# Kernel optimization log

Measured on AMD Instinct MI355X. Metric: run time of the kernel, lower is better.

Reference implementation:

```python
import jax, jax.numpy as jnp
import numpy as np

B, S, D, H = 2, 2048, 512, 8
DK = D // H  # 64
SCALE = (DK * 2) ** 0.5  # sqrt(2*d_k)


def setup_inputs() -> dict:
    key = jax.random.key(0)
    ks = jax.random.split(key, 10)
    f = lambda k, shape, s=1.0: jax.random.normal(k, shape, dtype=jnp.float32) * s
    return {
        "q_real": f(ks[0], (B, S, D)),
        "k_real": f(ks[1], (B, S, D)),
        "v_real": f(ks[2], (B, S, D)),
        "q_phase": f(ks[3], (B, S, D)),
        "k_phase": f(ks[4], (B, S, D)),
        "v_phase": f(ks[5], (B, S, D)),
        "w_q": f(ks[6], (D, D), 0.02),
        "w_k": f(ks[7], (D, D), 0.02),
        "w_v": f(ks[8], (D, D), 0.02),
        "w_o": f(ks[9], (D, D), 0.02),
        "mask": jnp.ones((B, S, S), dtype=jnp.int32),
    }


def _heads(x, w):
    # [B,S,D] @ [D,D] -> [B,H,S,DK]
    y = x @ w
    return y.reshape(B, -1, H, DK).transpose(0, 2, 1, 3)


def reference(q_real, k_real, v_real, q_phase, k_phase, v_phase,
              w_q, w_k, w_v, w_o, mask):
    qr, kr, vr = _heads(q_real, w_q), _heads(k_real, w_k), _heads(v_real, w_v)
    qp, kp, vp = _heads(q_phase, w_q), _heads(k_phase, w_k), _heads(v_phase, w_v)

    # complex-valued attention scores (continue_complex=False path)
    attn_real = jnp.einsum('bhqd,bhkd->bhqk', qr, kr) - jnp.einsum('bhqd,bhkd->bhqk', qp, kp)
    attn_phase = jnp.einsum('bhqd,bhkd->bhqk', qr, kp) + jnp.einsum('bhqd,bhkd->bhqk', qp, kr)

    attn = jnp.sqrt(attn_real * attn_real + attn_phase * attn_phase) / SCALE
    attn = jnp.where(mask[:, None, :, :] == 0, jnp.float32(-1e9), attn)
    attn = jax.nn.softmax(attn, axis=-1)

    xr = jnp.einsum('bhqk,bhkd->bhqd', attn, vr).transpose(0, 2, 1, 3).reshape(B, -1, D)
    xp = jnp.einsum('bhqk,bhkd->bhqd', attn, vp).transpose(0, 2, 1, 3).reshape(B, -1, D)
    return (xr @ w_o, xp @ w_o)
```

## Files before the change

### kernel.cpp

```cpp
#include <hip/hip_runtime.h>
#include <hip/hip_bf16.h>
#include <stdint.h>

#define Bb 2
#define Ss 2048
#define Dd 512
#define Hh 8
#define DKk 64

#define NROW 4096
#define MAT_E 2097152
#define W_E 262144

typedef __attribute__((ext_vector_type(8))) short short8;
typedef __attribute__((ext_vector_type(4))) float f32x4;

__device__ __forceinline__ unsigned short f2bf(float f) {
  union { float f; uint32_t u; } v; v.f = f;
  uint32_t u = v.u;
  uint32_t r = u + 0x7FFFu + ((u >> 16) & 1u);
  return (unsigned short)(r >> 16);
}

__device__ __forceinline__ void g2l16(const char* g, char* l) {
  __builtin_amdgcn_global_load_lds(
      (const __attribute__((address_space(1))) void*)g,
      (__attribute__((address_space(3))) void*)l, 16, 0, 0);
}

__global__ __launch_bounds__(256) void ck_cvt_in(
    const float* __restrict__ a0, const float* __restrict__ a1,
    const float* __restrict__ a2, const float* __restrict__ a3,
    const float* __restrict__ a4, const float* __restrict__ a5,
    unsigned short* __restrict__ out)
{
  int z = blockIdx.y;
  const float* src = z==0?a0: z==1?a1: z==2?a2: z==3?a3: z==4?a4: a5;
  unsigned short* dst = out + (size_t)z * MAT_E;
  int i = blockIdx.x * 256 + threadIdx.x;
  float4 v = ((const float4*)src)[i];
  unsigned short o[4] = {f2bf(v.x), f2bf(v.y), f2bf(v.z), f2bf(v.w)};
  *((uint2*)(dst + (size_t)i * 4)) = *((uint2*)o);
}

__global__ __launch_bounds__(256) void ck_cvt_wt(
    const float* __restrict__ w0, const float* __restrict__ w1,
    const float* __restrict__ w2, const float* __restrict__ w3,
    unsigned short* __restrict__ out)
{
  int z = blockIdx.y;
  const float* w = z==0?w0: z==1?w1: z==2?w2: w3;
  unsigned short* wt = out + (size_t)z * W_E;
  int t = blockIdx.x * 256 + threadIdx.x;
  int d = t >> 9, k = t & 511;
  wt[t] = f2bf(w[k * 512 + d]);
}

__global__ __launch_bounds__(256) void ck_mask_pack(
    const int* __restrict__ mask, unsigned long long* __restrict__ mb)
{
  size_t i = (size_t)blockIdx.x * 256 + threadIdx.x;
  int v = mask[i];
  unsigned long long bits = __ballot(v != 0);
  if ((threadIdx.x & 63) == 0) mb[i >> 6] = bits;
}

__device__ const size_t PROJ_OFF[6] = {0, 2097152, 8388608, 4194304, 6291456, 10485760};

__global__ __launch_bounds__(256) void ck_proj_gemm(
    const unsigned short* __restrict__ xb,
    const unsigned short* __restrict__ wt,
    unsigned short* __restrict__ proj)
{
  int z = blockIdx.z;
  const char* A = (const char*)(xb + (size_t)z * MAT_E);
  const char* W = (const char*)(wt + (size_t)(z % 3) * W_E);

  int tid = threadIdx.x;
  int wave = tid >> 6, lane = tid & 63;
  int lo = lane & 15, hi = lane >> 4;
  int wr = wave >> 1, wc = wave & 1;
  int m0 = blockIdx.x * 128, n0 = blockIdx.y * 128;

  __shared__ __align__(16) char smem[34816];
  char* A0 = smem;          char* A1 = smem + 8192;
  char* B0 = smem + 16384;  char* B1 = smem + 24576;

  int r0s = tid >> 2,        s0s = (tid & 3) ^ ((r0s >> 1) & 3);
  int c1  = 256 + tid;
  int r1s = c1 >> 2,         s1s = (c1 & 3) ^ ((r1s >> 1) & 3);
  int lb0 = wave * 1024;
  int lb1 = 4096 + wave * 1024;

  auto stage = [&](char* Ax, char* Bx, int k0) {
    g2l16(A + (size_t)(m0 + r0s) * 1024 + k0 * 2 + s0s * 16, Ax + lb0);
    g2l16(A + (size_t)(m0 + r1s) * 1024 + k0 * 2 + s1s * 16, Ax + lb1);
    g2l16(W + (size_t)(n0 + r0s) * 1024 + k0 * 2 + s0s * 16, Bx + lb0);
    g2l16(W + (size_t)(n0 + r1s) * 1024 + k0 * 2 + s1s * 16, Bx + lb1);
  };

  f32x4 acc[4][4];
  #pragma unroll
  for (int mf = 0; mf < 4; ++mf)
    #pragma unroll
    for (int nf = 0; nf < 4; ++nf) acc[mf][nf] = (f32x4){0.f, 0.f, 0.f, 0.f};

  int swz = (hi ^ ((lo >> 1) & 3)) * 16;

  auto compute = [&](const char* Ax, const char* Bx) {
    short8 af[4], bf[4];
    #pragma unroll
    for (int mf = 0; mf < 4; ++mf)
      af[mf] = *(const short8*)(Ax + (wr * 64 + mf * 16 + lo) * 64 + swz);
    #pragma unroll
    for (int nf = 0; nf < 4; ++nf)
      bf[nf] = *(const short8*)(Bx + (wc * 64 + nf * 16 + lo) * 64 + swz);
    #pragma unroll
    for (int mf = 0; mf < 4; ++mf)
      #pragma unroll
      for (int nf = 0; nf < 4; ++nf)
        acc[mf][nf] = __builtin_amdgcn_mfma_f32_16x16x32_bf16(af[mf], bf[nf], acc[mf][nf], 0, 0, 0);
  };

  stage(A0, B0, 0);
  __syncthreads();
  #pragma unroll 1
  for (int s = 0; s < 16; s += 2) {
    stage(A1, B1, (s + 1) * 32);
    compute(A0, B0);
    __syncthreads();
    if (s + 2 < 16) stage(A0, B0, (s + 2) * 32);
    compute(A1, B1);
    __syncthreads();
  }

  unsigned short* ep = (unsigned short*)smem;
  bool isV = (z == 2 || z == 5);
  #pragma unroll
  for (int mf = 0; mf < 4; ++mf)
    #pragma unroll
    for (int nf = 0; nf < 4; ++nf)
      #pragma unroll
      for (int r = 0; r < 4; ++r) {
        int grow = wr * 64 + mf * 16 + 4 * hi + r;
        int gcol = wc * 64 + nf * 16 + lo;
        unsigned short v = f2bf(acc[mf][nf][r]);
        if (isV) ep[gcol * 136 + grow] = v;
        else     ep[grow * 136 + gcol] = v;
      }
  __syncthreads();

  int b  = blockIdx.x >> 4;
  int s0 = (blockIdx.x * 128) & 2047;
  int h0 = blockIdx.y * 2;
  unsigned short* dst = proj + PROJ_OFF[z];
  #pragma unroll
  for (int i = 0; i < 8; ++i) {
    int cc = i * 256 + tid;
    int rr = cc >> 4, ch = cc & 15;
    uint4 d = *(const uint4*)(ep + rr * 136 + ch * 8);
    size_t off;
    if (isV)
      off = ((size_t)(b * 8 + h0 + (rr >> 6)) * 64 + (rr & 63)) * 2048 + s0 + ch * 8;
    else
      off = ((size_t)(b * 8 + h0 + (ch >> 3)) * 2048 + s0 + rr) * 64 + (ch & 7) * 8;
    *(uint4*)(dst + off) = d;
  }
}

__global__ __launch_bounds__(256) void ck_attn(
    const unsigned short* __restrict__ proj,
    const unsigned long long* __restrict__ mb,
    unsigned short* __restrict__ xout)
{
  const unsigned short* qr  = proj;
  const unsigned short* kr  = proj + 2097152;
  const unsigned short* qp  = proj + 4194304;
  const unsigned short* kp  = proj + 6291456;
  const unsigned short* vrt = proj + 8388608;
  const unsigned short* vpt = proj + 10485760;

  int bid = blockIdx.x;
  int swz = (bid & 7) * 64 + (bid >> 3);
  int qt = swz & 31, h = (swz >> 5) & 7, b = swz >> 8;

  int wave = threadIdx.x >> 6, lane = threadIdx.x & 63;
  int lo = lane & 15, hi = lane >> 4;
  int bh = b * Hh + h;
  size_t base = (size_t)bh * Ss * DKk;
  const char* Krb = (const char*)(kr + base);
  const char* Kpb = (const char*)(kp + base);
  const char* Vrb = (const char*)(vrt + base);
  const char* Vpb = (const char*)(vpt + base);
  const unsigned short* Qr = qr + base;
  const unsigned short* Qp = qp + base;

  __shared__ __align__(16) char kbuf[2][2][8192];
  __shared__ __align__(16) char vbuf[2][8192];
  __shared__ __align__(16) unsigned short plds[4 * 1024];
  char* pbase = (char*)plds + wave * 2048;

  int srow = wave * 8 + (lane >> 3);
  int scol = 16 * ((lane & 7) ^ ((lane >> 3) & 7));
  int lslot = wave * 1024 + lane * 16;

  #define STAGE_T(gbase, rstrideB, ltile)                                    \
    {                                                                        \
      g2l16((gbase) + (size_t)(srow) * (rstrideB) + scol, (ltile) + lslot);  \
      g2l16((gbase) + (size_t)(srow + 32) * (rstrideB) + scol,               \
            (ltile) + 4096 + lslot);                                         \
    }

  int q0 = qt * 64 + wave * 16;
  const unsigned long long* MBq = mb + ((size_t)b * Ss + q0) * 32;

  short8 fqr[2], fqp[2], fqpn[2];
  #pragma unroll
  for (int hf = 0; hf < 2; ++hf) {
    fqr[hf] = *(const short8*)(Qr + (size_t)(q0 + lo) * 64 + 32 * hf + 8 * hi);
    short8 p = *(const short8*)(Qp + (size_t)(q0 + lo) * 64 + 32 * hf + 8 * hi);
    fqp[hf] = p;
    union { short8 s; uint32_t u[4]; } pu; pu.s = p;
    #pragma unroll
    for (int i = 0; i < 4; ++i) pu.u[i] ^= 0x80008000u;
    fqpn[hf] = pu.s;
  }

  f32x4 o_r[4], o_p[4];
  float l_part[4];
  #pragma unroll
  for (int n = 0; n < 4; ++n) { o_r[n] = (f32x4){0,0,0,0}; o_p[n] = (f32x4){0,0,0,0}; }
  #pragma unroll
  for (int r = 0; r < 4; ++r) l_part[r] = 0.f;

  const float inv_scale = 0.08838834764831845f;

  STAGE_T(Krb, 128, kbuf[0][0]);
  STAGE_T(Kpb, 128, kbuf[0][1]);
  __syncthreads();

  int c = 0;
  for (int k0 = 0; k0 < Ss; k0 += 64) {
    STAGE_T(Vrb + (size_t)k0 * 2, 4096, vbuf[0]);
    STAGE_T(Vpb + (size_t)k0 * 2, 4096, vbuf[1]);
    if (k0 + 64 < Ss) {
      STAGE_T(Krb + (size_t)(k0 + 64) * 128, 128, kbuf[c ^ 1][0]);
      STAGE_T(Kpb + (size_t)(k0 + 64) * 128, 128, kbuf[c ^ 1][1]);
    }

    int wq = k0 >> 6;
    unsigned long long mrow[4];
    #pragma unroll
    for (int r = 0; r < 4; ++r) mrow[r] = MBq[(size_t)(4 * hi + r) * 32 + wq];
    unsigned long long andw = mrow[0] & mrow[1] & mrow[2] & mrow[3];
    bool need_mask = !__all((int)(andw == 0xFFFFFFFFFFFFFFFFull));

    const char* Kl = kbuf[c][0];
    const char* Pl = kbuf[c][1];
    f32x4 sre[4], sph[4];
    #pragma unroll
    for (int t = 0; t < 4; ++t) {
      int r0 = 16 * t + lo;
      int sw = (lo & 7) << 4;
      short8 bkr0 = *(const short8*)(Kl + r0 * 128 + ((16 * hi) ^ sw));
      short8 bkr1 = *(const short8*)(Kl + r0 * 128 + ((64 + 16 * hi) ^ sw));
      short8 bkp0 = *(const short8*)(Pl + r0 * 128 + ((16 * hi) ^ sw));
      short8 bkp1 = *(const short8*)(Pl + r0 * 128 + ((64 + 16 * hi) ^ sw));
      f32x4 re = (f32x4){0,0,0,0};
      re = __builtin_amdgcn_mfma_f32_16x16x32_bf16(fqr[0],  bkr0, re, 0,0,0);
      re = __builtin_amdgcn_mfma_f32_16x16x32_bf16(fqr[1],  bkr1, re, 0,0,0);
      re = __builtin_amdgcn_mfma_f32_16x16x32_bf16(fqpn[0], bkp0, re, 0,0,0);
      re = __builtin_amdgcn_mfma_f32_16x16x32_bf16(fqpn[1], bkp1, re, 0,0,0);
      f32x4 ph = (f32x4){0,0,0,0};
      ph = __builtin_amdgcn_mfma_f32_16x16x32_bf16(fqr[0],  bkp0, ph, 0,0,0);
      ph = __builtin_amdgcn_mfma_f32_16x16x32_bf16(fqr[1],  bkp1, ph, 0,0,0);
      ph = __builtin_amdgcn_mfma_f32_16x16x32_bf16(fqp[0],  bkr0, ph, 0,0,0);
      ph = __builtin_amdgcn_mfma_f32_16x16x32_bf16(fqp[1],  bkr1, ph, 0,0,0);
      sre[t] = re; sph[t] = ph;
    }

    float pvals[4][4];
    #pragma unroll
    for (int r = 0; r < 4; ++r) {
      unsigned long long sh = mrow[r] >> lo;
      #pragma unroll
      for (int t = 0; t < 4; ++t) {
        float re = sre[t][r], ph = sph[t][r];
        float v = __builtin_amdgcn_sqrtf(re * re + ph * ph) * inv_scale;
        if (need_mask)
          v = ((unsigned int)(sh >> (16 * t)) & 1u) ? v : -1e9f;
        float p = __expf(v);
        pvals[t][r] = p;
        l_part[r] += p;
      }
    }

    #pragma unroll
    for (int t = 0; t < 4; ++t) {
      #pragma unroll
      for (int r = 0; r < 4; ++r) {
        int row = 4 * hi + r;
        int off = row * 128 + ((((16 * t + lo) * 2) ^ ((row & 7) << 4)));
        *(unsigned short*)(pbase + off) = f2bf(pvals[t][r]);
      }
    }

    __syncthreads();

    short8 pa[2];
    #pragma unroll
    for (int hf = 0; hf < 2; ++hf) {
      int off = lo * 128 + (((hf * 64 + hi * 16)) ^ ((lo & 7) << 4));
      pa[hf] = *(const short8*)(pbase + off);
    }
    #pragma unroll
    for (int n = 0; n < 4; ++n) {
      int r0 = 16 * n + lo;
      int sw = (lo & 7) << 4;
      short8 bvr0 = *(const short8*)(vbuf[0] + r0 * 128 + ((16 * hi) ^ sw));
      short8 bvr1 = *(const short8*)(vbuf[0] + r0 * 128 + ((64 + 16 * hi) ^ sw));
      short8 bvp0 = *(const short8*)(vbuf[1] + r0 * 128 + ((16 * hi) ^ sw));
      short8 bvp1 = *(const short8*)(vbuf[1] + r0 * 128 + ((64 + 16 * hi) ^ sw));
      o_r[n] = __builtin_amdgcn_mfma_f32_16x16x32_bf16(pa[0], bvr0, o_r[n], 0,0,0);
      o_r[n] = __builtin_amdgcn_mfma_f32_16x16x32_bf16(pa[1], bvr1, o_r[n], 0,0,0);
      o_p[n] = __builtin_amdgcn_mfma_f32_16x16x32_bf16(pa[0], bvp0, o_p[n], 0,0,0);
      o_p[n] = __builtin_amdgcn_mfma_f32_16x16x32_bf16(pa[1], bvp1, o_p[n], 0,0,0);
    }

    __syncthreads();
    c ^= 1;
  }

  #pragma unroll
  for (int r = 0; r < 4; ++r) {
    float v = l_part[r];
    v += __shfl_xor(v, 1);
    v += __shfl_xor(v, 2);
    v += __shfl_xor(v, 4);
    v += __shfl_xor(v, 8);
    l_part[r] = v;
  }
  float invl[4];
  #pragma unroll
  for (int r = 0; r < 4; ++r) invl[r] = 1.f / l_part[r];
  #pragma unroll
  for (int n = 0; n < 4; ++n) {
    #pragma unroll
    for (int r = 0; r < 4; ++r) {
      int q = q0 + 4 * hi + r;
      size_t off = (size_t)(b * Ss + q) * Dd + h * 64 + 16 * n + lo;
      xout[off]         = f2bf(o_r[n][r] * invl[r]);
      xout[MAT_E + off] = f2bf(o_p[n][r] * invl[r]);
    }
  }
  #undef STAGE_T
}

__global__ __launch_bounds__(256) void ck_out_gemm(
    const unsigned short* __restrict__ x,
    const unsigned short* __restrict__ wot,
    float* __restrict__ out)
{
  int z = blockIdx.z;
  const char* A = (const char*)(x + (size_t)z * MAT_E);
  const char* W = (const char*)wot;
  float* O = out + (size_t)z * MAT_E;

  int tid = threadIdx.x;
  int wave = tid >> 6, lane = tid & 63;
  int lo = lane & 15, hi = lane >> 4;
  int wr = wave >> 1, wc = wave & 1;
  int m0 = blockIdx.x * 128, n0 = blockIdx.y * 128;

  __shared__ __align__(16) char smem[32768];
  char* A0 = smem;          char* A1 = smem + 8192;
  char* B0 = smem + 16384;  char* B1 = smem + 24576;

  int r0s = tid >> 2,  s0s = (tid & 3) ^ ((r0s >> 1) & 3);
  int c1  = 256 + tid;
  int r1s = c1 >> 2,   s1s = (c1 & 3) ^ ((r1s >> 1) & 3);
  int lb0 = wave * 1024;
  int lb1 = 4096 + wave * 1024;

  auto stage = [&](char* Ax, char* Bx, int k0) {
    g2l16(A + (size_t)(m0 + r0s) * 1024 + k0 * 2 + s0s * 16, Ax + lb0);
    g2l16(A + (size_t)(m0 + r1s) * 1024 + k0 * 2 + s1s * 16, Ax + lb1);
    g2l16(W + (size_t)(n0 + r0s) * 1024 + k0 * 2 + s0s * 16, Bx + lb0);
    g2l16(W + (size_t)(n0 + r1s) * 1024 + k0 * 2 + s1s * 16, Bx + lb1);
  };

  f32x4 acc[4][4];
  #pragma unroll
  for (int mf = 0; mf < 4; ++mf)
    #pragma unroll
    for (int nf = 0; nf < 4; ++nf) acc[mf][nf] = (f32x4){0.f, 0.f, 0.f, 0.f};

  int swz = (hi ^ ((lo >> 1) & 3)) * 16;

  auto compute = [&](const char* Ax, const char* Bx) {
    short8 af[4], bf[4];
    #pragma unroll
    for (int mf = 0; mf < 4; ++mf)
      af[mf] = *(const short8*)(Ax + (wr * 64 + mf * 16 + lo) * 64 + swz);
    #pragma unroll
    for (int nf = 0; nf < 4; ++nf)
      bf[nf] = *(const short8*)(Bx + (wc * 64 + nf * 16 + lo) * 64 + swz);
    #pragma unroll
    for (int mf = 0; mf < 4; ++mf)
      #pragma unroll
      for (int nf = 0; nf < 4; ++nf)
        acc[mf][nf] = __builtin_amdgcn_mfma_f32_16x16x32_bf16(af[mf], bf[nf], acc[mf][nf], 0, 0, 0);
  };

  stage(A0, B0, 0);
  __syncthreads();
  #pragma unroll 1
  for (int s = 0; s < 16; s += 2) {
    stage(A1, B1, (s + 1) * 32);
    compute(A0, B0);
    __syncthreads();
    if (s + 2 < 16) stage(A0, B0, (s + 2) * 32);
    compute(A1, B1);
    __syncthreads();
  }

  #pragma unroll
  for (int mf = 0; mf < 4; ++mf)
    #pragma unroll
    for (int nf = 0; nf < 4; ++nf)
      #pragma unroll
      for (int r = 0; r < 4; ++r) {
        int m = m0 + wr * 64 + mf * 16 + 4 * hi + r;
        int n = n0 + wc * 64 + nf * 16 + lo;
        O[(size_t)m * 512 + n] = acc[mf][nf][r];
      }
}

extern "C" void kernel_launch(void* const* d_in, const int* in_sizes, int n_in,
                              void* d_out, int out_size, void* d_ws, size_t ws_size,
                              hipStream_t stream) {
  const float* q_real  = (const float*)d_in[0];
  const float* k_real  = (const float*)d_in[1];
  const float* v_real  = (const float*)d_in[2];
  const float* q_phase = (const float*)d_in[3];
  const float* k_phase = (const float*)d_in[4];
  const float* v_phase = (const float*)d_in[5];
  const float* w_q     = (const float*)d_in[6];
  const float* w_k     = (const float*)d_in[7];
  const float* w_v     = (const float*)d_in[8];
  const float* w_o     = (const float*)d_in[9];
  const int*   mask    = (const int*)d_in[10];
  float* out = (float*)d_out;

  unsigned short* ws   = (unsigned short*)d_ws;
  unsigned short* XB   = ws;
  unsigned short* WT   = ws + 6 * (size_t)MAT_E;
  unsigned short* PROJ = WT + 4 * (size_t)W_E;
  unsigned short* XOUT = PROJ + 6 * (size_t)MAT_E;
  unsigned long long* MB = (unsigned long long*)XB;

  ck_cvt_in  <<<dim3(2048, 6), 256, 0, stream>>>(q_real, k_real, v_real,
                                                 q_phase, k_phase, v_phase, XB);
  ck_cvt_wt  <<<dim3(1024, 4), 256, 0, stream>>>(w_q, w_k, w_v, w_o, WT);
  ck_proj_gemm<<<dim3(32, 4, 6), 256, 0, stream>>>(XB, WT, PROJ);
  ck_mask_pack<<<dim3(32768), 256, 0, stream>>>(mask, MB);
  ck_attn    <<<dim3(512), 256, 0, stream>>>(PROJ, MB, XOUT);
  ck_out_gemm<<<dim3(32, 4, 2), 256, 0, stream>>>(XOUT, WT + 3 * (size_t)W_E, out);
}
```

Measured before the change: 263.5 us.

## Halve attention key tile and cap registers for four blocks per CU

Cuts the attention key tile from 64 to 32 rows per iteration and halves the K double-buffer in LDS, while V is still staged every 64 keys and its two halves are consumed on alternating iterations. Launch bounds now request four blocks per CU, and per-iteration register arrays shrink, to lower register and LDS pressure and raise occupancy. The cost is twice as many loop iterations and barriers, plus smaller MFMA batches between syncs.

```diff
diff --git a/kernel.cpp b/kernel.cpp
--- a/kernel.cpp
+++ b/kernel.cpp
@@ -168,7 +168,7 @@
   }
 }
 
-__global__ __launch_bounds__(256) void ck_attn(
+__global__ __launch_bounds__(256, 4) void ck_attn(
     const unsigned short* __restrict__ proj,
     const unsigned long long* __restrict__ mb,
     unsigned short* __restrict__ xout)
@@ -184,7 +184,8 @@
   int swz = (bid & 7) * 64 + (bid >> 3);
   int qt = swz & 31, h = (swz >> 5) & 7, b = swz >> 8;
 
-  int wave = threadIdx.x >> 6, lane = threadIdx.x & 63;
+  int tid = threadIdx.x;
+  int wave = tid >> 6, lane = tid & 63;
   int lo = lane & 15, hi = lane >> 4;
   int bh = b * Hh + h;
   size_t base = (size_t)bh * Ss * DKk;
@@ -195,21 +196,14 @@
   const unsigned short* Qr = qr + base;
   const unsigned short* Qp = qp + base;
 
-  __shared__ __align__(16) char kbuf[2][2][8192];
+  __shared__ __align__(16) char kbuf[2][2][4096];
   __shared__ __align__(16) char vbuf[2][8192];
   __shared__ __align__(16) unsigned short plds[4 * 1024];
   char* pbase = (char*)plds + wave * 2048;
 
-  int srow = wave * 8 + (lane >> 3);
-  int scol = 16 * ((lane & 7) ^ ((lane >> 3) & 7));
-  int lslot = wave * 1024 + lane * 16;
-
-  #define STAGE_T(gbase, rstrideB, ltile)                                    \
-    {                                                                        \
-      g2l16((gbase) + (size_t)(srow) * (rstrideB) + scol, (ltile) + lslot);  \
-      g2l16((gbase) + (size_t)(srow + 32) * (rstrideB) + scol,               \
-            (ltile) + 4096 + lslot);                                         \
-    }
+  int srow = tid >> 3;
+  int scol = 16 * ((tid & 7) ^ ((tid >> 3) & 7));
+  int dstc = tid * 16;
 
   int q0 = qt * 64 + wave * 16;
   const unsigned long long* MBq = mb + ((size_t)b * Ss + q0) * 32;
@@ -235,31 +229,45 @@
 
   const float inv_scale = 0.08838834764831845f;
 
-  STAGE_T(Krb, 128, kbuf[0][0]);
-  STAGE_T(Kpb, 128, kbuf[0][1]);
+  g2l16(Krb + (size_t)srow * 128 + scol, kbuf[0][0] + dstc);
+  g2l16(Kpb + (size_t)srow * 128 + scol, kbuf[0][1] + dstc);
   __syncthreads();
 
+  unsigned long long mrow64[4];
   int c = 0;
-  for (int k0 = 0; k0 < Ss; k0 += 64) {
-    STAGE_T(Vrb + (size_t)k0 * 2, 4096, vbuf[0]);
-    STAGE_T(Vpb + (size_t)k0 * 2, 4096, vbuf[1]);
-    if (k0 + 64 < Ss) {
-      STAGE_T(Krb + (size_t)(k0 + 64) * 128, 128, kbuf[c ^ 1][0]);
-      STAGE_T(Kpb + (size_t)(k0 + 64) * 128, 128, kbuf[c ^ 1][1]);
-    }
-
-    int wq = k0 >> 6;
-    unsigned long long mrow[4];
-    #pragma unroll
-    for (int r = 0; r < 4; ++r) mrow[r] = MBq[(size_t)(4 * hi + r) * 32 + wq];
-    unsigned long long andw = mrow[0] & mrow[1] & mrow[2] & mrow[3];
-    bool need_mask = !__all((int)(andw == 0xFFFFFFFFFFFFFFFFull));
+  #pragma unroll 1
+  for (int k0 = 0; k0 < Ss; k0 += 32) {
+    if ((k0 & 32) == 0) {
+      #pragma unroll
+      for (int j = 0; j < 2; ++j) {
+        g2l16(Vrb + (size_t)(j * 32 + srow) * 4096 + k0 * 2 + scol,
+              vbuf[0] + j * 4096 + dstc);
+        g2l16(Vpb + (size_t)(j * 32 + srow) * 4096 + k0 * 2 + scol,
+              vbuf[1] + j * 4096 + dstc);
+      }
+      #pragma unroll
+      for (int r = 0; r < 4; ++r)
+        mrow64[r] = MBq[(size_t)(4 * hi + r) * 32 + (k0 >> 6)];
+    }
+    if (k0 + 32 < Ss) {
+      g2l16(Krb + (size_t)(k0 + 32 + srow) * 128 + scol, kbuf[c ^ 1][0] + dstc);
+      g2l16(Kpb + (size_t)(k0 + 32 + srow) * 128 + scol, kbuf[c ^ 1][1] + dstc);
+    }
+
+    unsigned mbits[4];
+    unsigned andm = 0xFFFFFFFFu;
+    #pragma unroll
+    for (int r = 0; r < 4; ++r) {
+      mbits[r] = (unsigned)(mrow64[r] >> (k0 & 32));
+      andm &= mbits[r];
+    }
+    bool need_mask = !__all((int)(andm == 0xFFFFFFFFu));
 
     const char* Kl = kbuf[c][0];
     const char* Pl = kbuf[c][1];
-    f32x4 sre[4], sph[4];
-    #pragma unroll
-    for (int t = 0; t < 4; ++t) {
+    f32x4 sre[2], sph[2];
+    #pragma unroll
+    for (int t = 0; t < 2; ++t) {
       int r0 = 16 * t + lo;
       int sw = (lo & 7) << 4;
       short8 bkr0 = *(const short8*)(Kl + r0 * 128 + ((16 * hi) ^ sw));
@@ -279,16 +287,16 @@
       sre[t] = re; sph[t] = ph;
     }
 
-    float pvals[4][4];
+    float pvals[2][4];
     #pragma unroll
     for (int r = 0; r < 4; ++r) {
-      unsigned long long sh = mrow[r] >> lo;
-      #pragma unroll
-      for (int t = 0; t < 4; ++t) {
+      unsigned sh = mbits[r] >> lo;
+      #pragma unroll
+      for (int t = 0; t < 2; ++t) {
         float re = sre[t][r], ph = sph[t][r];
         float v = __builtin_amdgcn_sqrtf(re * re + ph * ph) * inv_scale;
         if (need_mask)
-          v = ((unsigned int)(sh >> (16 * t)) & 1u) ? v : -1e9f;
+          v = ((sh >> (16 * t)) & 1u) ? v : -1e9f;
         float p = __expf(v);
         pvals[t][r] = p;
         l_part[r] += p;
@@ -296,7 +304,7 @@
     }
 
     #pragma unroll
-    for (int t = 0; t < 4; ++t) {
+    for (int t = 0; t < 2; ++t) {
       #pragma unroll
       for (int r = 0; r < 4; ++r) {
         int row = 4 * hi + r;
@@ -307,24 +315,16 @@
 
     __syncthreads();
 
-    short8 pa[2];
-    #pragma unroll
-    for (int hf = 0; hf < 2; ++hf) {
-      int off = lo * 128 + (((hf * 64 + hi * 16)) ^ ((lo & 7) << 4));
-      pa[hf] = *(const short8*)(pbase + off);
-    }
+    int vhb = (k0 & 32) * 2;
+    short8 pa = *(const short8*)(pbase + lo * 128 + ((hi * 16) ^ ((lo & 7) << 4)));
     #pragma unroll
     for (int n = 0; n < 4; ++n) {
       int r0 = 16 * n + lo;
       int sw = (lo & 7) << 4;
-      short8 bvr0 = *(const short8*)(vbuf[0] + r0 * 128 + ((16 * hi) ^ sw));
-      short8 bvr1 = *(const short8*)(vbuf[0] + r0 * 128 + ((64 + 16 * hi) ^ sw));
-      short8 bvp0 = *(const short8*)(vbuf[1] + r0 * 128 + ((16 * hi) ^ sw));
-      short8 bvp1 = *(const short8*)(vbuf[1] + r0 * 128 + ((64 + 16 * hi) ^ sw));
-      o_r[n] = __builtin_amdgcn_mfma_f32_16x16x32_bf16(pa[0], bvr0, o_r[n], 0,0,0);
-      o_r[n] = __builtin_amdgcn_mfma_f32_16x16x32_bf16(pa[1], bvr1, o_r[n], 0,0,0);
-      o_p[n] = __builtin_amdgcn_mfma_f32_16x16x32_bf16(pa[0], bvp0, o_p[n], 0,0,0);
-      o_p[n] = __builtin_amdgcn_mfma_f32_16x16x32_bf16(pa[1], bvp1, o_p[n], 0,0,0);
+      short8 bvr = *(const short8*)(vbuf[0] + r0 * 128 + ((vhb + 16 * hi) ^ sw));
+      short8 bvp = *(const short8*)(vbuf[1] + r0 * 128 + ((vhb + 16 * hi) ^ sw));
+      o_r[n] = __builtin_amdgcn_mfma_f32_16x16x32_bf16(pa, bvr, o_r[n], 0,0,0);
+      o_p[n] = __builtin_amdgcn_mfma_f32_16x16x32_bf16(pa, bvp, o_p[n], 0,0,0);
     }
 
     __syncthreads();
@@ -353,7 +353,6 @@
       xout[MAT_E + off] = f2bf(o_p[n][r] * invl[r]);
     }
   }
-  #undef STAGE_T
 }
 
 __global__ __launch_bounds__(256) void ck_out_gemm(
```

New measurement: 273.4 us. 1.04x slower.
